# Kernel tuning notes

Measured on AMD Instinct MI355X. Metric: run time of the kernel, lower is better.

## Reference

```python
import jax, jax.numpy as jnp
import numpy as np

N_NODES = 50000
N_EDGES = 400000
NUM_FEATS = 128
LATENT_DIM_Y = 64
HIDDEN = 512
OUT = 2


def gcn_conv(x, edge_index, W, b, num_nodes):
    """PyG GCNConv: add self-loops, symmetric normalization, x @ W then scatter-add."""
    x = x @ W  # [N, out_ch]
    loop = jnp.arange(num_nodes)
    row = jnp.concatenate([edge_index[0], loop])  # source nodes
    col = jnp.concatenate([edge_index[1], loop])  # target nodes
    deg = jax.ops.segment_sum(jnp.ones_like(col, dtype=x.dtype), col, num_segments=num_nodes)
    dinv = jnp.where(deg > 0, jax.lax.rsqrt(deg), 0.0)
    norm = dinv[row] * dinv[col]  # [E+N]
    msgs = norm[:, None] * x[row]  # gather source features, scale
    out = jax.ops.segment_sum(msgs, col, num_segments=num_nodes)
    return out + b


def setup_inputs() -> dict:
    key = jax.random.key(0)
    k1, k2, k3, k4, k5, k6, k7 = jax.random.split(key, 7)
    in_ch = NUM_FEATS + LATENT_DIM_Y
    inputs = {
        "edge_index": jax.random.randint(k1, (2, N_EDGES), 0, N_NODES),
        "X": jax.random.normal(k2, (N_NODES, NUM_FEATS), dtype=jnp.float32),
        "u_Y": jax.random.normal(k3, (N_NODES, LATENT_DIM_Y), dtype=jnp.float32),
        "W1": jax.random.normal(k4, (in_ch, HIDDEN), dtype=jnp.float32) / np.sqrt(in_ch),
        "b1": jnp.zeros((HIDDEN,), dtype=jnp.float32),
        "W2": jax.random.normal(k5, (HIDDEN, OUT), dtype=jnp.float32) / np.sqrt(HIDDEN),
        "b2": jnp.zeros((OUT,), dtype=jnp.float32),
    }
    return inputs


def reference(edge_index, X, u_Y, W1, b1, W2, b2):
    latent = jnp.concatenate([u_Y, X], axis=1)  # [N, latent+feats]
    h = jax.nn.relu(gcn_conv(latent, edge_index, W1, b1, N_NODES))
    y = gcn_conv(h, edge_index, W2, b2, N_NODES)
    # nn.Softmax() on a 2D tensor defaults to dim=1
    return jax.nn.softmax(y, axis=1)
```

## Files before the change

kernel.cpp:

```cpp
#include <hip/hip_runtime.h>

#define N_NODES 50000
#define N_EDGES 400000
#define FEATS   128
#define LAT     64
#define IN_CH   192
#define HID     512
#define MB      64
#define CAP     32

#define E4       100000
#define SC_BLKS  391
#define CVT_BLKS 4688
#define W1_BLKS  384

typedef __attribute__((ext_vector_type(8))) short bf16x8;
typedef __attribute__((ext_vector_type(4))) float f32x4;

static inline int cdiv(int a, int b) { return (a + b - 1) / b; }

__device__ __forceinline__ unsigned short f2bf(float f) {
    unsigned int u = __float_as_uint(f);
    u = (u + 0x7fffu + ((u >> 16) & 1u)) >> 16;
    return (unsigned short)u;
}
__device__ __forceinline__ unsigned int pack2bf(float lo, float hi) {
    return (unsigned int)f2bf(lo) | ((unsigned int)f2bf(hi) << 16);
}
__device__ __forceinline__ float bf_lo(unsigned int u) {
    return __uint_as_float(u << 16);
}
__device__ __forceinline__ float bf_hi(unsigned int u) {
    return __uint_as_float(u & 0xffff0000u);
}

__global__ __launch_bounds__(256) void
k_front(const int* __restrict__ ei, int* __restrict__ cursor, int* __restrict__ csr_src,
        const float* __restrict__ uY, const float* __restrict__ X,
        unsigned short* __restrict__ latent,
        const float* __restrict__ W1, unsigned short* __restrict__ W1f) {
    int bid = blockIdx.x;
    if (bid < SC_BLKS) {
        int i4 = bid * 256 + threadIdx.x;
        if (i4 < E4) {
            int4 r = ((const int4*)ei)[i4];
            int4 c = ((const int4*)(ei + N_EDGES))[i4];
            int p0 = atomicAdd(&cursor[c.x], 1);
            int p1 = atomicAdd(&cursor[c.y], 1);
            int p2 = atomicAdd(&cursor[c.z], 1);
            int p3 = atomicAdd(&cursor[c.w], 1);
            csr_src[c.x * CAP + p0] = r.x;
            csr_src[c.y * CAP + p1] = r.y;
            csr_src[c.z * CAP + p2] = r.z;
            csr_src[c.w * CAP + p3] = r.w;
        }
    } else if (bid < SC_BLKS + CVT_BLKS) {
        int idx = (bid - SC_BLKS) * 256 + threadIdx.x;
        if (idx < N_NODES * 24) {
            int i = idx / 24, q = idx % 24;
            const float4* uY4 = (const float4*)uY;
            const float4* X4  = (const float4*)X;
            float4 v0, v1;
            if (q < 8) {
                v0 = uY4[i * 16 + 2 * q];
                v1 = uY4[i * 16 + 2 * q + 1];
            } else {
                v0 = X4[i * 32 + 2 * (q - 8)];
                v1 = X4[i * 32 + 2 * (q - 8) + 1];
            }
            uint4 o;
            o.x = pack2bf(v0.x, v0.y);
            o.y = pack2bf(v0.z, v0.w);
            o.z = pack2bf(v1.x, v1.y);
            o.w = pack2bf(v1.z, v1.w);
            ((uint4*)latent)[idx] = o;
        }
    } else {
        int idx = (bid - SC_BLKS - CVT_BLKS) * 256 + threadIdx.x;
        if (idx < IN_CH * HID) {
            int k = idx / HID, n = idx % HID;
            int ntile = n >> 4, nn = n & 15;
            int kc = k >> 5, q = (k >> 3) & 3, j = k & 7;
            int dst = (((ntile * 6 + kc) * 64 + q * 16 + nn) << 3) + j;
            W1f[dst] = f2bf(W1[idx]);
        }
    }
}

__device__ __forceinline__ void fma6(float* acc, float wt,
                                     unsigned int A, unsigned int B, unsigned int C) {
    acc[0] = fmaf(wt, bf_lo(A), acc[0]);
    acc[1] = fmaf(wt, bf_hi(A), acc[1]);
    acc[2] = fmaf(wt, bf_lo(B), acc[2]);
    acc[3] = fmaf(wt, bf_hi(B), acc[3]);
    acc[4] = fmaf(wt, bf_lo(C), acc[4]);
    acc[5] = fmaf(wt, bf_hi(C), acc[5]);
}

__global__ __launch_bounds__(256) void
k_gather_agg(const int* __restrict__ cursor, const int* __restrict__ csr_src,
             const unsigned short* __restrict__ latent, unsigned short* __restrict__ agg) {
    int tid = threadIdx.x;
    int w   = blockIdx.x * 8 + (tid >> 5);
    int il  = tid & 31;
    if (w >= N_NODES) return;
    int lbase = tid & 32;
    const char* __restrict__ Lb = (const char*)latent;

    int deg = cursor[w];
    int raw = csr_src[w * CAP + max(il - 1, 0)];
    int rl  = (il == 0 || il - 1 >= deg) ? w : min(max(raw, 0), N_NODES - 1);
    int dl  = cursor[rl];
    float di = rsqrtf((float)(deg + 1));
    float wl = (il == 0) ? di * di
             : ((il - 1 < deg) ? di * rsqrtf((float)(dl + 1)) : 0.f);
    int off_l = rl * 384;

    int R = (deg + 8) & ~7;

    float acc[6];
#pragma unroll
    for (int i = 0; i < 6; ++i) acc[i] = 0.f;

    auto LD = [&](int t, float& wt, uint2& U, unsigned int& C) {
        wt = __shfl(wl, lbase + t);
        int off = __shfl(off_l, lbase + t);
        const char* p = Lb + off;
        U = *(const uint2*)(p + 8 * il);
        C = *(const unsigned int*)(p + 256 + 4 * il);
    };

    float w0, w1, w2, w3, w4, w5, w6, w7;
    uint2 U0, U1, U2, U3, U4, U5, U6, U7;
    unsigned int C0, C1, C2, C3, C4, C5, C6, C7;
    LD(0, w0, U0, C0); LD(1, w1, U1, C1); LD(2, w2, U2, C2); LD(3, w3, U3, C3);
    LD(4, w4, U4, C4); LD(5, w5, U5, C5); LD(6, w6, U6, C6); LD(7, w7, U7, C7);
    int t = 0;
    for (; t + 15 < R; t += 8) {
        float v0, v1, v2, v3, v4, v5, v6, v7;
        uint2 V0, V1, V2, V3, V4, V5, V6, V7;
        unsigned int D0, D1, D2, D3, D4, D5, D6, D7;
        LD(t + 8,  v0, V0, D0); LD(t + 9,  v1, V1, D1);
        LD(t + 10, v2, V2, D2); LD(t + 11, v3, V3, D3);
        LD(t + 12, v4, V4, D4); LD(t + 13, v5, V5, D5);
        LD(t + 14, v6, V6, D6); LD(t + 15, v7, V7, D7);
        fma6(acc, w0, U0.x, U0.y, C0); fma6(acc, w1, U1.x, U1.y, C1);
        fma6(acc, w2, U2.x, U2.y, C2); fma6(acc, w3, U3.x, U3.y, C3);
        fma6(acc, w4, U4.x, U4.y, C4); fma6(acc, w5, U5.x, U5.y, C5);
        fma6(acc, w6, U6.x, U6.y, C6); fma6(acc, w7, U7.x, U7.y, C7);
        w0 = v0; U0 = V0; C0 = D0;  w1 = v1; U1 = V1; C1 = D1;
        w2 = v2; U2 = V2; C2 = D2;  w3 = v3; U3 = V3; C3 = D3;
        w4 = v4; U4 = V4; C4 = D4;  w5 = v5; U5 = V5; C5 = D5;
        w6 = v6; U6 = V6; C6 = D6;  w7 = v7; U7 = V7; C7 = D7;
    }
    fma6(acc, w0, U0.x, U0.y, C0); fma6(acc, w1, U1.x, U1.y, C1);
    fma6(acc, w2, U2.x, U2.y, C2); fma6(acc, w3, U3.x, U3.y, C3);
    fma6(acc, w4, U4.x, U4.y, C4); fma6(acc, w5, U5.x, U5.y, C5);
    fma6(acc, w6, U6.x, U6.y, C6); fma6(acc, w7, U7.x, U7.y, C7);

    unsigned int* op = (unsigned int*)agg + (size_t)w * 96;
    uint2 o;
    o.x = pack2bf(acc[0], acc[1]);
    o.y = pack2bf(acc[2], acc[3]);
    *((uint2*)op + il) = o;
    op[64 + il] = pack2bf(acc[4], acc[5]);
}

__global__ __launch_bounds__(256, 2) void
k_gemm_mfma(const unsigned short* __restrict__ agg, const unsigned short* __restrict__ W1f,
            const float* __restrict__ b1, const float* __restrict__ W2,
            float* __restrict__ y_pre) {
    __shared__ unsigned short Af[MB * IN_CH];
    __shared__ float red[4][MB][2];

    int t  = threadIdx.x;
    int m0 = blockIdx.x * MB;

    {
        const uint4* src = (const uint4*)agg;
        for (int idx = t; idx < MB * 24; idx += 256) {
            int row = idx / 24, c = idx % 24;
            int g = m0 + row;
            uint4 v = make_uint4(0u, 0u, 0u, 0u);
            if (g < N_NODES) v = src[(size_t)g * 24 + c];
            int mt = row >> 4, m = row & 15, kc = c >> 2, q = c & 3;
            ((uint4*)Af)[(mt * 6 + kc) * 64 + q * 16 + m] = v;
        }
    }
    __syncthreads();

    int wid = t >> 6, lane = t & 63;
    int nl = lane & 15, q = lane >> 4;

    float b1v[8], w2a[8], w2b[8];
#pragma unroll
    for (int nt = 0; nt < 8; ++nt) {
        int n = wid * 128 + nt * 16 + nl;
        b1v[nt] = b1[n];
        w2a[nt] = W2[n * 2 + 0];
        w2b[nt] = W2[n * 2 + 1];
    }

    f32x4 acc[4][8];
#pragma unroll
    for (int mt = 0; mt < 4; ++mt)
#pragma unroll
        for (int nt = 0; nt < 8; ++nt) acc[mt][nt] = (f32x4){0.f, 0.f, 0.f, 0.f};

    const bf16x8* Afv = (const bf16x8*)Af;
    const bf16x8* Bv  = (const bf16x8*)W1f;
#pragma unroll
    for (int kc = 0; kc < 6; ++kc) {
        bf16x8 a[4];
#pragma unroll
        for (int mt = 0; mt < 4; ++mt) a[mt] = Afv[(mt * 6 + kc) * 64 + lane];
#pragma unroll
        for (int nt = 0; nt < 8; ++nt) {
            bf16x8 b = Bv[((wid * 8 + nt) * 6 + kc) * 64 + lane];
#pragma unroll
            for (int mt = 0; mt < 4; ++mt)
                acc[mt][nt] = __builtin_amdgcn_mfma_f32_16x16x32_bf16(a[mt], b, acc[mt][nt], 0, 0, 0);
        }
    }

#pragma unroll
    for (int mt = 0; mt < 4; ++mt) {
#pragma unroll
        for (int r = 0; r < 4; ++r) {
            float p0 = 0.f, p1 = 0.f;
#pragma unroll
            for (int nt = 0; nt < 8; ++nt) {
                float h = fmaxf(acc[mt][nt][r] + b1v[nt], 0.f);
                p0 = fmaf(h, w2a[nt], p0);
                p1 = fmaf(h, w2b[nt], p1);
            }
#pragma unroll
            for (int off = 1; off < 16; off <<= 1) {
                p0 += __shfl_xor(p0, off);
                p1 += __shfl_xor(p1, off);
            }
            if (nl == 0) {
                int row = mt * 16 + q * 4 + r;
                red[wid][row][0] = p0;
                red[wid][row][1] = p1;
            }
        }
    }
    __syncthreads();
    if (t < MB * 2) {
        int row = t >> 1, j = t & 1;
        float s = red[0][row][j] + red[1][row][j] + red[2][row][j] + red[3][row][j];
        int g = m0 + row;
        if (g < N_NODES) y_pre[g * 2 + j] = s;
    }
}

__global__ __launch_bounds__(256) void
k_gather_y(const int* __restrict__ cursor, const int* __restrict__ csr_src,
           const float* __restrict__ y_pre, const float* __restrict__ b2,
           float* __restrict__ out) {
    int i  = blockIdx.x * 32 + (threadIdx.x >> 3);
    int l8 = threadIdx.x & 7;
    if (i >= N_NODES) return;
    const float2* __restrict__ yp = (const float2*)y_pre;

    int jlo = i * CAP;
    int deg  = cursor[i];
    int rawe = csr_src[jlo + max(l8 - 1, 0)];
    int raw2 = csr_src[jlo + l8 + 7];
    int raw1 = (l8 == 0) ? i : rawe;
    int r1 = min(max(raw1, 0), N_NODES - 1);
    int r2 = min(max(raw2, 0), N_NODES - 1);
    int d1 = cursor[r1], d2 = cursor[r2];
    float2 v1 = yp[r1];

    float di = rsqrtf((float)(deg + 1));
    float w1 = (l8 == 0) ? di
             : ((l8 - 1 < deg) ? rsqrtf((float)(d1 + 1)) : 0.f);
    float a0 = w1 * v1.x, a1 = w1 * v1.y;
    if (deg > 7) {
        float2 v2 = yp[r2];
        float w2 = (l8 + 7 < deg) ? rsqrtf((float)(d2 + 1)) : 0.f;
        a0 = fmaf(w2, v2.x, a0);
        a1 = fmaf(w2, v2.y, a1);
        for (int e = 15 + l8; e < deg; e += 8) {
            int r = csr_src[jlo + e];
            float wt = rsqrtf((float)(cursor[r] + 1));
            float2 v = yp[r];
            a0 = fmaf(wt, v.x, a0);
            a1 = fmaf(wt, v.y, a1);
        }
    }
#pragma unroll
    for (int off = 1; off < 8; off <<= 1) {
        a0 += __shfl_xor(a0, off);
        a1 += __shfl_xor(a1, off);
    }
    if (l8 == 0) {
        float ya = di * a0 + b2[0];
        float yb = di * a1 + b2[1];
        float mx = fmaxf(ya, yb);
        float e0 = expf(ya - mx);
        float e1 = expf(yb - mx);
        float inv = 1.0f / (e0 + e1);
        out[i * 2 + 0] = e0 * inv;
        out[i * 2 + 1] = e1 * inv;
    }
}


extern "C" void kernel_launch(void* const* d_in, const int* in_sizes, int n_in,
                              void* d_out, int out_size, void* d_ws, size_t ws_size,
                              hipStream_t stream) {
    const int*   ei = (const int*)d_in[0];
    const float* X  = (const float*)d_in[1];
    const float* uY = (const float*)d_in[2];
    const float* W1 = (const float*)d_in[3];
    const float* b1 = (const float*)d_in[4];
    const float* W2 = (const float*)d_in[5];
    const float* b2 = (const float*)d_in[6];
    float* out = (float*)d_out;

    char* ws = (char*)d_ws;
    auto carve = [&](size_t bytes) {
        char* p = ws;
        ws += (bytes + 255) & ~size_t(255);
        return p;
    };
    int*   cursor    = (int*)carve(N_NODES * sizeof(int));
    int*   csr_src   = (int*)carve((size_t)N_NODES * CAP * sizeof(int));
    unsigned short* latent = (unsigned short*)carve((size_t)N_NODES * IN_CH * 2);
    unsigned short* aggb   = (unsigned short*)carve((size_t)N_NODES * IN_CH * 2);
    unsigned short* W1f    = (unsigned short*)carve((size_t)IN_CH * HID * 2);
    float* y_pre     = (float*)carve((size_t)N_NODES * 2 * sizeof(float));

    hipMemsetAsync(cursor, 0, N_NODES * sizeof(int), stream);

    k_front     <<<SC_BLKS + CVT_BLKS + W1_BLKS, 256, 0, stream>>>(
                      ei, cursor, csr_src, uY, X, latent, W1, W1f);

    k_gather_agg<<<cdiv(N_NODES, 8), 256, 0, stream>>>(
                      cursor, csr_src, latent, aggb);

    k_gemm_mfma <<<cdiv(N_NODES, MB), 256, 0, stream>>>(aggb, W1f, b1, W2, y_pre);

    k_gather_y  <<<cdiv(N_NODES, 32), 256, 0, stream>>>(
                      cursor, csr_src, y_pre, b2, out);
}
```

Baseline: 172.6 us.

## Fuse neighbor aggregation into MFMA GEMM kernel via shared-memory staging

Measured after the change: 177.4 us. +2.8%, slower.

```diff
diff --git a/kernel.cpp b/kernel.cpp
--- a/kernel.cpp
+++ b/kernel.cpp
@@ -6,7 +6,7 @@
 #define LAT     64
 #define IN_CH   192
 #define HID     512
-#define MB      64
+#define MB      32
 #define CAP     32
 
 #define E4       100000
@@ -97,99 +97,91 @@
     acc[5] = fmaf(wt, bf_hi(C), acc[5]);
 }
 
-__global__ __launch_bounds__(256) void
-k_gather_agg(const int* __restrict__ cursor, const int* __restrict__ csr_src,
-             const unsigned short* __restrict__ latent, unsigned short* __restrict__ agg) {
+__global__ __launch_bounds__(256, 2) void
+k_fused(const int* __restrict__ cursor, const int* __restrict__ csr_src,
+        const unsigned short* __restrict__ latent,
+        const unsigned short* __restrict__ W1f,
+        const float* __restrict__ b1, const float* __restrict__ W2,
+        float* __restrict__ y_pre) {
+    __shared__ unsigned short Af[MB * IN_CH];
+    __shared__ float red[4][MB][2];
+
     int tid = threadIdx.x;
-    int w   = blockIdx.x * 8 + (tid >> 5);
+    int m0  = blockIdx.x * MB;
+    int hw  = tid >> 5;
     int il  = tid & 31;
-    if (w >= N_NODES) return;
     int lbase = tid & 32;
     const char* __restrict__ Lb = (const char*)latent;
 
-    int deg = cursor[w];
-    int raw = csr_src[w * CAP + max(il - 1, 0)];
-    int rl  = (il == 0 || il - 1 >= deg) ? w : min(max(raw, 0), N_NODES - 1);
-    int dl  = cursor[rl];
-    float di = rsqrtf((float)(deg + 1));
-    float wl = (il == 0) ? di * di
-             : ((il - 1 < deg) ? di * rsqrtf((float)(dl + 1)) : 0.f);
-    int off_l = rl * 384;
-
-    int R = (deg + 8) & ~7;
-
-    float acc[6];
-#pragma unroll
-    for (int i = 0; i < 6; ++i) acc[i] = 0.f;
-
-    auto LD = [&](int t, float& wt, uint2& U, unsigned int& C) {
-        wt = __shfl(wl, lbase + t);
-        int off = __shfl(off_l, lbase + t);
-        const char* p = Lb + off;
-        U = *(const uint2*)(p + 8 * il);
-        C = *(const unsigned int*)(p + 256 + 4 * il);
-    };
-
-    float w0, w1, w2, w3, w4, w5, w6, w7;
-    uint2 U0, U1, U2, U3, U4, U5, U6, U7;
-    unsigned int C0, C1, C2, C3, C4, C5, C6, C7;
-    LD(0, w0, U0, C0); LD(1, w1, U1, C1); LD(2, w2, U2, C2); LD(3, w3, U3, C3);
-    LD(4, w4, U4, C4); LD(5, w5, U5, C5); LD(6, w6, U6, C6); LD(7, w7, U7, C7);
-    int t = 0;
-    for (; t + 15 < R; t += 8) {
-        float v0, v1, v2, v3, v4, v5, v6, v7;
-        uint2 V0, V1, V2, V3, V4, V5, V6, V7;
-        unsigned int D0, D1, D2, D3, D4, D5, D6, D7;
-        LD(t + 8,  v0, V0, D0); LD(t + 9,  v1, V1, D1);
-        LD(t + 10, v2, V2, D2); LD(t + 11, v3, V3, D3);
-        LD(t + 12, v4, V4, D4); LD(t + 13, v5, V5, D5);
-        LD(t + 14, v6, V6, D6); LD(t + 15, v7, V7, D7);
+#pragma unroll
+    for (int k = 0; k < 4; ++k) {
+        int row = hw * 4 + k;
+        int w   = min(m0 + row, N_NODES - 1);
+        int deg = cursor[w];
+        int raw = csr_src[w * CAP + max(il - 1, 0)];
+        int rl  = (il == 0 || il - 1 >= deg) ? w : min(max(raw, 0), N_NODES - 1);
+        int dl  = cursor[rl];
+        float di = rsqrtf((float)(deg + 1));
+        float wl = (il == 0) ? di * di
+                 : ((il - 1 < deg) ? di * rsqrtf((float)(dl + 1)) : 0.f);
+        int off_l = rl * 384;
+
+        int R = (deg + 8) & ~7;
+
+        float acc[6];
+#pragma unroll
+        for (int i = 0; i < 6; ++i) acc[i] = 0.f;
+
+        auto LD = [&](int t, float& wt, uint2& U, unsigned int& C) {
+            wt = __shfl(wl, lbase + t);
+            int off = __shfl(off_l, lbase + t);
+            const char* p = Lb + off;
+            U = *(const uint2*)(p + 8 * il);
+            C = *(const unsigned int*)(p + 256 + 4 * il);
+        };
+
+        float w0, w1, w2, w3, w4, w5, w6, w7;
+        uint2 U0, U1, U2, U3, U4, U5, U6, U7;
+        unsigned int C0, C1, C2, C3, C4, C5, C6, C7;
+        LD(0, w0, U0, C0); LD(1, w1, U1, C1); LD(2, w2, U2, C2); LD(3, w3, U3, C3);
+        LD(4, w4, U4, C4); LD(5, w5, U5, C5); LD(6, w6, U6, C6); LD(7, w7, U7, C7);
+        int t = 0;
+        for (; t + 15 < R; t += 8) {
+            float v0, v1, v2, v3, v4, v5, v6, v7;
+            uint2 V0, V1, V2, V3, V4, V5, V6, V7;
+            unsigned int D0, D1, D2, D3, D4, D5, D6, D7;
+            LD(t + 8,  v0, V0, D0); LD(t + 9,  v1, V1, D1);
+            LD(t + 10, v2, V2, D2); LD(t + 11, v3, V3, D3);
+            LD(t + 12, v4, V4, D4); LD(t + 13, v5, V5, D5);
+            LD(t + 14, v6, V6, D6); LD(t + 15, v7, V7, D7);
+            fma6(acc, w0, U0.x, U0.y, C0); fma6(acc, w1, U1.x, U1.y, C1);
+            fma6(acc, w2, U2.x, U2.y, C2); fma6(acc, w3, U3.x, U3.y, C3);
+            fma6(acc, w4, U4.x, U4.y, C4); fma6(acc, w5, U5.x, U5.y, C5);
+            fma6(acc, w6, U6.x, U6.y, C6); fma6(acc, w7, U7.x, U7.y, C7);
+            w0 = v0; U0 = V0; C0 = D0;  w1 = v1; U1 = V1; C1 = D1;
+            w2 = v2; U2 = V2; C2 = D2;  w3 = v3; U3 = V3; C3 = D3;
+            w4 = v4; U4 = V4; C4 = D4;  w5 = v5; U5 = V5; C5 = D5;
+            w6 = v6; U6 = V6; C6 = D6;  w7 = v7; U7 = V7; C7 = D7;
+        }
         fma6(acc, w0, U0.x, U0.y, C0); fma6(acc, w1, U1.x, U1.y, C1);
         fma6(acc, w2, U2.x, U2.y, C2); fma6(acc, w3, U3.x, U3.y, C3);
         fma6(acc, w4, U4.x, U4.y, C4); fma6(acc, w5, U5.x, U5.y, C5);
         fma6(acc, w6, U6.x, U6.y, C6); fma6(acc, w7, U7.x, U7.y, C7);
-        w0 = v0; U0 = V0; C0 = D0;  w1 = v1; U1 = V1; C1 = D1;
-        w2 = v2; U2 = V2; C2 = D2;  w3 = v3; U3 = V3; C3 = D3;
-        w4 = v4; U4 = V4; C4 = D4;  w5 = v5; U5 = V5; C5 = D5;
-        w6 = v6; U6 = V6; C6 = D6;  w7 = v7; U7 = V7; C7 = D7;
-    }
-    fma6(acc, w0, U0.x, U0.y, C0); fma6(acc, w1, U1.x, U1.y, C1);
-    fma6(acc, w2, U2.x, U2.y, C2); fma6(acc, w3, U3.x, U3.y, C3);
-    fma6(acc, w4, U4.x, U4.y, C4); fma6(acc, w5, U5.x, U5.y, C5);
-    fma6(acc, w6, U6.x, U6.y, C6); fma6(acc, w7, U7.x, U7.y, C7);
-
-    unsigned int* op = (unsigned int*)agg + (size_t)w * 96;
-    uint2 o;
-    o.x = pack2bf(acc[0], acc[1]);
-    o.y = pack2bf(acc[2], acc[3]);
-    *((uint2*)op + il) = o;
-    op[64 + il] = pack2bf(acc[4], acc[5]);
-}
-
-__global__ __launch_bounds__(256, 2) void
-k_gemm_mfma(const unsigned short* __restrict__ agg, const unsigned short* __restrict__ W1f,
-            const float* __restrict__ b1, const float* __restrict__ W2,
-            float* __restrict__ y_pre) {
-    __shared__ unsigned short Af[MB * IN_CH];
-    __shared__ float red[4][MB][2];
-
-    int t  = threadIdx.x;
-    int m0 = blockIdx.x * MB;
-
-    {
-        const uint4* src = (const uint4*)agg;
-        for (int idx = t; idx < MB * 24; idx += 256) {
-            int row = idx / 24, c = idx % 24;
-            int g = m0 + row;
-            uint4 v = make_uint4(0u, 0u, 0u, 0u);
-            if (g < N_NODES) v = src[(size_t)g * 24 + c];
-            int mt = row >> 4, m = row & 15, kc = c >> 2, q = c & 3;
-            ((uint4*)Af)[(mt * 6 + kc) * 64 + q * 16 + m] = v;
-        }
+
+        int mt = row >> 4, m = row & 15;
+        int c1 = il >> 1;
+        int idx1 = (mt * 6 + (c1 >> 2)) * 64 + (c1 & 3) * 16 + m;
+        uint2 o;
+        o.x = pack2bf(acc[0], acc[1]);
+        o.y = pack2bf(acc[2], acc[3]);
+        *(uint2*)((char*)Af + idx1 * 16 + (il & 1) * 8) = o;
+        int c2 = 16 + (il >> 2);
+        int idx2 = (mt * 6 + (c2 >> 2)) * 64 + (c2 & 3) * 16 + m;
+        *(unsigned int*)((char*)Af + idx2 * 16 + (il & 3) * 4) = pack2bf(acc[4], acc[5]);
     }
     __syncthreads();
 
-    int wid = t >> 6, lane = t & 63;
+    int wid = tid >> 6, lane = tid & 63;
     int nl = lane & 15, q = lane >> 4;
 
     float b1v[8], w2a[8], w2b[8];
@@ -201,36 +193,36 @@
         w2b[nt] = W2[n * 2 + 1];
     }
 
-    f32x4 acc[4][8];
-#pragma unroll
-    for (int mt = 0; mt < 4; ++mt)
-#pragma unroll
-        for (int nt = 0; nt < 8; ++nt) acc[mt][nt] = (f32x4){0.f, 0.f, 0.f, 0.f};
+    f32x4 gacc[2][8];
+#pragma unroll
+    for (int mt = 0; mt < 2; ++mt)
+#pragma unroll
+        for (int nt = 0; nt < 8; ++nt) gacc[mt][nt] = (f32x4){0.f, 0.f, 0.f, 0.f};
 
     const bf16x8* Afv = (const bf16x8*)Af;
     const bf16x8* Bv  = (const bf16x8*)W1f;
 #pragma unroll
     for (int kc = 0; kc < 6; ++kc) {
-        bf16x8 a[4];
-#pragma unroll
-        for (int mt = 0; mt < 4; ++mt) a[mt] = Afv[(mt * 6 + kc) * 64 + lane];
+        bf16x8 a[2];
+#pragma unroll
+        for (int mt = 0; mt < 2; ++mt) a[mt] = Afv[(mt * 6 + kc) * 64 + lane];
 #pragma unroll
         for (int nt = 0; nt < 8; ++nt) {
             bf16x8 b = Bv[((wid * 8 + nt) * 6 + kc) * 64 + lane];
 #pragma unroll
-            for (int mt = 0; mt < 4; ++mt)
-                acc[mt][nt] = __builtin_amdgcn_mfma_f32_16x16x32_bf16(a[mt], b, acc[mt][nt], 0, 0, 0);
-        }
-    }
-
-#pragma unroll
-    for (int mt = 0; mt < 4; ++mt) {
+            for (int mt = 0; mt < 2; ++mt)
+                gacc[mt][nt] = __builtin_amdgcn_mfma_f32_16x16x32_bf16(a[mt], b, gacc[mt][nt], 0, 0, 0);
+        }
+    }
+
+#pragma unroll
+    for (int mt = 0; mt < 2; ++mt) {
 #pragma unroll
         for (int r = 0; r < 4; ++r) {
             float p0 = 0.f, p1 = 0.f;
 #pragma unroll
             for (int nt = 0; nt < 8; ++nt) {
-                float h = fmaxf(acc[mt][nt][r] + b1v[nt], 0.f);
+                float h = fmaxf(gacc[mt][nt][r] + b1v[nt], 0.f);
                 p0 = fmaf(h, w2a[nt], p0);
                 p1 = fmaf(h, w2b[nt], p1);
             }
@@ -247,8 +239,8 @@
         }
     }
     __syncthreads();
-    if (t < MB * 2) {
-        int row = t >> 1, j = t & 1;
+    if (tid < MB * 2) {
+        int row = tid >> 1, j = tid & 1;
         float s = red[0][row][j] + red[1][row][j] + red[2][row][j] + red[3][row][j];
         int g = m0 + row;
         if (g < N_NODES) y_pre[g * 2 + j] = s;
@@ -330,20 +322,17 @@
     int*   cursor    = (int*)carve(N_NODES * sizeof(int));
     int*   csr_src   = (int*)carve((size_t)N_NODES * CAP * sizeof(int));
     unsigned short* latent = (unsigned short*)carve((size_t)N_NODES * IN_CH * 2);
-    unsigned short* aggb   = (unsigned short*)carve((size_t)N_NODES * IN_CH * 2);
     unsigned short* W1f    = (unsigned short*)carve((size_t)IN_CH * HID * 2);
     float* y_pre     = (float*)carve((size_t)N_NODES * 2 * sizeof(float));
 
     hipMemsetAsync(cursor, 0, N_NODES * sizeof(int), stream);
 
-    k_front     <<<SC_BLKS + CVT_BLKS + W1_BLKS, 256, 0, stream>>>(
-                      ei, cursor, csr_src, uY, X, latent, W1, W1f);
-
-    k_gather_agg<<<cdiv(N_NODES, 8), 256, 0, stream>>>(
-                      cursor, csr_src, latent, aggb);
-
-    k_gemm_mfma <<<cdiv(N_NODES, MB), 256, 0, stream>>>(aggb, W1f, b1, W2, y_pre);
-
-    k_gather_y  <<<cdiv(N_NODES, 32), 256, 0, stream>>>(
-                      cursor, csr_src, y_pre, b2, out);
-}
+    k_front   <<<SC_BLKS + CVT_BLKS + W1_BLKS, 256, 0, stream>>>(
+                    ei, cursor, csr_src, uY, X, latent, W1, W1f);
+
+    k_fused   <<<cdiv(N_NODES, MB), 256, 0, stream>>>(
+                    cursor, csr_src, latent, W1f, b1, W2, y_pre);
+
+    k_gather_y<<<cdiv(N_NODES, 32), 256, 0, stream>>>(
+                    cursor, csr_src, y_pre, b2, out);
+}
```
